# Performance work log

Measured on AMD Instinct MI355X. Metric: run time of the kernel, lower is better.

The kernel has to match this reference:

```python
import jax, jax.numpy as jnp
import numpy as np

B, N = 8192, 4096
P = Q = R = S = 64            # square Monarch blocks: sqrt(N)
K = N // P                    # 64
L = N * Q // (P * R)          # 64


def setup_inputs() -> dict:
    key = jax.random.key(0)
    kx, k1, k2 = jax.random.split(key, 3)
    x = jax.random.normal(kx, (B, N), dtype=jnp.float32)
    w1_bfly = jax.random.normal(k1, (K, Q, P), dtype=jnp.float32)
    w2_bfly = jax.random.normal(k2, (L, S, R), dtype=jnp.float32)
    return {"x": x, "w1_bfly": w1_bfly, "w2_bfly": w2_bfly}


def reference(x, w1_bfly, w2_bfly):
    # x: (B, n); w1: (k, q, p); w2: (l, s, r); k*p = n, l*r = k*q
    b, n = x.shape
    k, q, p = w1_bfly.shape
    l, s, r = w2_bfly.shape
    # stage 1: block-diagonal bmm -> (b, k, q)
    out1 = jnp.einsum('bkp,kqp->bkq', x.reshape(b, k, p), w1_bfly)
    # permutation between stages: (b, k*q) -> (b, r, l) -> (b, l, r)
    out1 = out1.reshape(b, r, l).transpose(0, 2, 1)
    # stage 2: block-diagonal bmm -> (b, l, s)
    out2 = jnp.einsum('blr,lsr->bls', out1, w2_bfly)
    # final permute: (b, l, s) -> (b, s, l) -> (b, s*l)
    return out2.transpose(0, 2, 1).reshape(b, s * l)
```

## Files before the change

kernel.cpp:

```cpp
#include <hip/hip_runtime.h>


typedef __bf16 bf16x8 __attribute__((ext_vector_type(8)));
typedef float  float4v __attribute__((ext_vector_type(4)));

__global__ __launch_bounds__(256)
void cvt_weights(const float* __restrict__ w1, const float* __restrict__ w2,
                 __bf16* __restrict__ wb) {
    const int i = (blockIdx.x * 256 + threadIdx.x) * 8;
    float4v a = *(const float4v*)(w1 + i);
    float4v b = *(const float4v*)(w1 + i + 4);
    bf16x8 v;
    v[0]=(__bf16)a[0]; v[1]=(__bf16)a[1]; v[2]=(__bf16)a[2]; v[3]=(__bf16)a[3];
    v[4]=(__bf16)b[0]; v[5]=(__bf16)b[1]; v[6]=(__bf16)b[2]; v[7]=(__bf16)b[3];
    *(bf16x8*)(wb + i) = v;
    a = *(const float4v*)(w2 + i);
    b = *(const float4v*)(w2 + i + 4);
    v[0]=(__bf16)a[0]; v[1]=(__bf16)a[1]; v[2]=(__bf16)a[2]; v[3]=(__bf16)a[3];
    v[4]=(__bf16)b[0]; v[5]=(__bf16)b[1]; v[6]=(__bf16)b[2]; v[7]=(__bf16)b[3];
    *(bf16x8*)(wb + 262144 + i) = v;
}

__global__ __launch_bounds__(512, 2)
void monarch_fused(const float* __restrict__ x,
                   const __bf16* __restrict__ w1b,
                   const __bf16* __restrict__ w2b,
                   float* __restrict__ out)
{
    __shared__ __align__(16) __bf16 Y[16 * 16 * 64];

    const int tid  = threadIdx.x;
    const int wid  = tid >> 6;
    const int lane = tid & 63;
    const int m    = lane & 15;
    const int quad = lane >> 4;
    const int b0   = blockIdx.x * 16;

    bf16x8 xa[8][2];
    {
        const float* xp = x + (long)(b0 + m) * 4096 + wid * 512 + quad * 8;
        #pragma unroll
        for (int j = 0; j < 8; ++j) {
            #pragma unroll
            for (int h = 0; h < 2; ++h) {
                float4v lo = *(const float4v*)(xp + j * 64 + h * 32);
                float4v hi = *(const float4v*)(xp + j * 64 + h * 32 + 4);
                bf16x8 v;
                v[0]=(__bf16)lo[0]; v[1]=(__bf16)lo[1]; v[2]=(__bf16)lo[2]; v[3]=(__bf16)lo[3];
                v[4]=(__bf16)hi[0]; v[5]=(__bf16)hi[1]; v[6]=(__bf16)hi[2]; v[7]=(__bf16)hi[3];
                xa[j][h] = v;
            }
        }
    }

    const int lg = wid >> 1;
    const int sh = wid & 1;

    for (int qc = 0; qc < 4; ++qc) {
        float4v acc[8];
        #pragma unroll
        for (int j = 0; j < 8; ++j) {
            const int k = wid * 8 + j;
            const __bf16* w1p = w1b + ((k * 64 + qc * 16 + m) * 64) + quad * 8;
            bf16x8 bb0 = *(const bf16x8*)(w1p);
            bf16x8 bb1 = *(const bf16x8*)(w1p + 32);
            float4v c = {0.f, 0.f, 0.f, 0.f};
            c = __builtin_amdgcn_mfma_f32_16x16x32_bf16(xa[j][0], bb0, c, 0, 0, 0);
            c = __builtin_amdgcn_mfma_f32_16x16x32_bf16(xa[j][1], bb1, c, 0, 0, 0);
            acc[j] = c;
        }

        __syncthreads();

        #pragma unroll
        for (int reg = 0; reg < 4; ++reg) {
            const int bl = quad * 4 + reg;
            const int cs = wid ^ (m & 7) ^ (bl & 7);
            bf16x8 v;
            #pragma unroll
            for (int j = 0; j < 8; ++j) v[j] = (__bf16)acc[j][reg];
            *(bf16x8*)(&Y[((bl * 16 + m) * 8 + cs) * 8]) = v;
        }
        __syncthreads();

        float4v acc2[4][2];
        #pragma unroll
        for (int li = 0; li < 4; ++li)
            #pragma unroll
            for (int st = 0; st < 2; ++st) acc2[li][st] = (float4v){0.f, 0.f, 0.f, 0.f};

        #pragma unroll
        for (int h = 0; h < 2; ++h) {
            #pragma unroll
            for (int li = 0; li < 4; ++li) {
                const int ll = lg * 4 + li;
                const int l  = qc * 16 + ll;
                const int kc = h * 4 + quad;
                const int cs = kc ^ (ll & 7) ^ (m & 7);
                bf16x8 a2 = *(const bf16x8*)(&Y[((m * 16 + ll) * 8 + cs) * 8]);
                const __bf16* w2p = w2b + (l * 64) * 64 + h * 32 + quad * 8;
                #pragma unroll
                for (int st = 0; st < 2; ++st) {
                    const int s = (sh * 2 + st) * 16 + m;
                    bf16x8 b2 = *(const bf16x8*)(w2p + s * 64);
                    acc2[li][st] = __builtin_amdgcn_mfma_f32_16x16x32_bf16(a2, b2, acc2[li][st], 0, 0, 0);
                }
            }
        }

        #pragma unroll
        for (int st = 0; st < 2; ++st) {
            #pragma unroll
            for (int reg = 0; reg < 4; ++reg) {
                float4v v;
                #pragma unroll
                for (int li = 0; li < 4; ++li) v[li] = acc2[li][st][reg];
                float* dst = out + (long)(b0 + quad * 4 + reg) * 4096
                                 + ((sh * 2 + st) * 16 + m) * 64 + qc * 16 + lg * 4;
                *(float4v*)dst = v;
            }
        }
    }
}

extern "C" void kernel_launch(void* const* d_in, const int* in_sizes, int n_in,
                              void* d_out, int out_size, void* d_ws, size_t ws_size,
                              hipStream_t stream) {
    const float* x  = (const float*)d_in[0];
    const float* w1 = (const float*)d_in[1];
    const float* w2 = (const float*)d_in[2];
    float* out = (float*)d_out;
    __bf16* wb = (__bf16*)d_ws;

    hipLaunchKernelGGL(cvt_weights, dim3(128), dim3(256), 0, stream, w1, w2, wb);
    hipLaunchKernelGGL(monarch_fused, dim3(8192 / 16), dim3(512), 0, stream,
                       x, wb, wb + 262144, out);
}
```

Baseline: 341.1 us.

## Process 32 q-columns per phase to halve block-wide barriers in Monarch kernel

The q dimension is now processed in two phases of 32 columns instead of four phases of 16. The shared staging buffer doubles to 64 KB, and each wave computes all four s-tiles for its own four l values. This cuts the number of __syncthreads rounds per block and raises per-wave work between barriers. In exchange it uses more LDS and accumulator registers, which may lower occupancy below the two-blocks-per-CU launch bound.

```diff
diff --git a/kernel.cpp b/kernel.cpp
--- a/kernel.cpp
+++ b/kernel.cpp
@@ -27,7 +27,7 @@
                    const __bf16* __restrict__ w2b,
                    float* __restrict__ out)
 {
-    __shared__ __align__(16) __bf16 Y[16 * 16 * 64];
+    __shared__ __align__(16) __bf16 Y[16 * 32 * 64];
 
     const int tid  = threadIdx.x;
     const int wid  = tid >> 6;
@@ -53,70 +53,70 @@
         }
     }
 
-    const int lg = wid >> 1;
-    const int sh = wid & 1;
-
-    for (int qc = 0; qc < 4; ++qc) {
-        float4v acc[8];
-        #pragma unroll
-        for (int j = 0; j < 8; ++j) {
-            const int k = wid * 8 + j;
-            const __bf16* w1p = w1b + ((k * 64 + qc * 16 + m) * 64) + quad * 8;
-            bf16x8 bb0 = *(const bf16x8*)(w1p);
-            bf16x8 bb1 = *(const bf16x8*)(w1p + 32);
-            float4v c = {0.f, 0.f, 0.f, 0.f};
-            c = __builtin_amdgcn_mfma_f32_16x16x32_bf16(xa[j][0], bb0, c, 0, 0, 0);
-            c = __builtin_amdgcn_mfma_f32_16x16x32_bf16(xa[j][1], bb1, c, 0, 0, 0);
-            acc[j] = c;
-        }
-
-        __syncthreads();
+    for (int qh = 0; qh < 2; ++qh) {
+        if (qh) __syncthreads();
 
         #pragma unroll
-        for (int reg = 0; reg < 4; ++reg) {
-            const int bl = quad * 4 + reg;
-            const int cs = wid ^ (m & 7) ^ (bl & 7);
-            bf16x8 v;
+        for (int qt = 0; qt < 2; ++qt) {
+            float4v acc[8];
             #pragma unroll
-            for (int j = 0; j < 8; ++j) v[j] = (__bf16)acc[j][reg];
-            *(bf16x8*)(&Y[((bl * 16 + m) * 8 + cs) * 8]) = v;
+            for (int j = 0; j < 8; ++j) {
+                const int k = wid * 8 + j;
+                const int q = qh * 32 + qt * 16 + m;
+                const __bf16* w1p = w1b + ((k * 64 + q) * 64) + quad * 8;
+                bf16x8 bb0 = *(const bf16x8*)(w1p);
+                bf16x8 bb1 = *(const bf16x8*)(w1p + 32);
+                float4v c = {0.f, 0.f, 0.f, 0.f};
+                c = __builtin_amdgcn_mfma_f32_16x16x32_bf16(xa[j][0], bb0, c, 0, 0, 0);
+                c = __builtin_amdgcn_mfma_f32_16x16x32_bf16(xa[j][1], bb1, c, 0, 0, 0);
+                acc[j] = c;
+            }
+            #pragma unroll
+            for (int reg = 0; reg < 4; ++reg) {
+                const int bl   = quad * 4 + reg;
+                const int qloc = qt * 16 + m;
+                const int cs   = wid ^ (qloc & 7) ^ (bl & 7);
+                bf16x8 v;
+                #pragma unroll
+                for (int j = 0; j < 8; ++j) v[j] = (__bf16)acc[j][reg];
+                *(bf16x8*)(&Y[((bl * 32 + qloc) * 8 + cs) * 8]) = v;
+            }
         }
         __syncthreads();
 
-        float4v acc2[4][2];
+        float4v acc2[4][4];
         #pragma unroll
         for (int li = 0; li < 4; ++li)
             #pragma unroll
-            for (int st = 0; st < 2; ++st) acc2[li][st] = (float4v){0.f, 0.f, 0.f, 0.f};
+            for (int st = 0; st < 4; ++st) acc2[li][st] = (float4v){0.f, 0.f, 0.f, 0.f};
 
         #pragma unroll
         for (int h = 0; h < 2; ++h) {
             #pragma unroll
             for (int li = 0; li < 4; ++li) {
-                const int ll = lg * 4 + li;
-                const int l  = qc * 16 + ll;
-                const int kc = h * 4 + quad;
-                const int cs = kc ^ (ll & 7) ^ (m & 7);
-                bf16x8 a2 = *(const bf16x8*)(&Y[((m * 16 + ll) * 8 + cs) * 8]);
+                const int qloc = wid * 4 + li;
+                const int l    = qh * 32 + qloc;
+                const int kc   = h * 4 + quad;
+                const int cs   = kc ^ (qloc & 7) ^ (m & 7);
+                bf16x8 a2 = *(const bf16x8*)(&Y[((m * 32 + qloc) * 8 + cs) * 8]);
                 const __bf16* w2p = w2b + (l * 64) * 64 + h * 32 + quad * 8;
                 #pragma unroll
-                for (int st = 0; st < 2; ++st) {
-                    const int s = (sh * 2 + st) * 16 + m;
-                    bf16x8 b2 = *(const bf16x8*)(w2p + s * 64);
+                for (int st = 0; st < 4; ++st) {
+                    bf16x8 b2 = *(const bf16x8*)(w2p + (st * 16 + m) * 64);
                     acc2[li][st] = __builtin_amdgcn_mfma_f32_16x16x32_bf16(a2, b2, acc2[li][st], 0, 0, 0);
                 }
             }
         }
 
         #pragma unroll
-        for (int st = 0; st < 2; ++st) {
+        for (int st = 0; st < 4; ++st) {
             #pragma unroll
             for (int reg = 0; reg < 4; ++reg) {
                 float4v v;
                 #pragma unroll
                 for (int li = 0; li < 4; ++li) v[li] = acc2[li][st][reg];
                 float* dst = out + (long)(b0 + quad * 4 + reg) * 4096
-                                 + ((sh * 2 + st) * 16 + m) * 64 + qc * 16 + lg * 4;
+                                 + (st * 16 + m) * 64 + qh * 32 + wid * 4;
                 *(float4v*)dst = v;
             }
         }
```

Result: no change. 342.9 us (+0.5%).
